# Kernel tuning notes

Measured on AMD Instinct MI355X. Metric: run time of the kernel, lower is better.

Reference implementation:

```python
import jax, jax.numpy as jnp
import numpy as np

N, K, D, E = 20000, 63, 50, 300  # nodes, neighbors per node, hidden dim, entity input dim


def setup_inputs() -> dict:
    key = jax.random.key(0)
    ks = jax.random.split(key, 12)
    inp = {
        "query_emb": jax.random.normal(ks[0], (N, D), jnp.float32),
        "entity_emb": jax.random.normal(ks[1], (N, E), jnp.float32),
        "neighbor_embs": jax.random.normal(ks[2], (N, K, D), jnp.float32),
        "neighbor_scores": jax.random.uniform(ks[3], (N, K + 1), jnp.float32),
        # learned parameters (xavier-ish scale)
        "Wp": jax.random.normal(ks[4], (D, E), jnp.float32) * (1.0 / np.sqrt(E)),
        "bp": jnp.zeros((D,), jnp.float32),
        "Wbil": jax.random.normal(ks[5], (D, D, D), jnp.float32) * (1.0 / D),
        "bbil": jnp.zeros((D,), jnp.float32),
        "Wg": jax.random.normal(ks[6], (D, D), jnp.float32) * (1.0 / np.sqrt(D)),
        "g_bias": jnp.zeros((D,), jnp.float32),
        "Wr": jax.random.normal(ks[7], (1, D), jnp.float32) * (1.0 / np.sqrt(D)),
        "br": jnp.zeros((1,), jnp.float32),
    }
    return inp


def reference(query_emb, entity_emb, neighbor_embs, neighbor_scores,
              Wp, bp, Wbil, bbil, Wg, g_bias, Wr, br):
    # entity projection: [N,E] -> [N,D]
    ent = entity_emb @ Wp.T + bp
    # bilinear query-entity interaction: node[n,o] = q[n,i] Wbil[o,i,j] ent[n,j] + bbil[o]
    node = jnp.einsum('ni,oij,nj->no', query_emb, Wbil, ent) + bbil  # [N,D]
    # ragged neighbor texts = K paraembeds + the node's own embedding (uniform K here)
    texts = jnp.concatenate([neighbor_embs, node[:, None, :]], axis=1)  # [N,K+1,D]
    # GRN: project neighbors, scale by attention scores, sum over neighbors
    # (dropout p=0.01 is identity in eval mode)
    proj = jnp.einsum('nkd,od->nko', texts, Wg)           # [N,K+1,D]
    agg = jnp.einsum('nko,nk->no', proj, neighbor_scores)  # attention-weighted scatter-sum
    feats = jax.nn.elu(agg + g_bias)                       # bias + ELU activation
    # rank score head: [N,D] -> [N,1]
    return feats @ Wr.T + br
```

## Files before the change

kernel.cpp:

```cpp
#include <hip/hip_runtime.h>
#include <math.h>

#define NN 20000
typedef unsigned int uint;
typedef unsigned short ushort;
typedef __attribute__((ext_vector_type(8))) short bf16x8;
typedef __attribute__((ext_vector_type(4))) float f32x4;

union U8 { uint4 u; bf16x8 v; };

__device__ __forceinline__ ushort f2b(float x) {
    uint u = __float_as_uint(x);
    return (ushort)((u + 0x7FFFu + ((u >> 16) & 1u)) >> 16);
}
__device__ __forceinline__ float b2f(ushort b) {
    return __uint_as_float(((uint)b) << 16);
}
__device__ __forceinline__ uint pkmul(uint e2, float qv) {
    float lo = __uint_as_float(e2 << 16) * qv;
    float hi = __uint_as_float(e2 & 0xFFFF0000u) * qv;
    uint ul = (__float_as_uint(lo) + 0x8000u) >> 16;
    uint uh = (__float_as_uint(hi) + 0x8000u) & 0xFFFF0000u;
    return ul | uh;
}

__global__ __launch_bounds__(256) void kPrep(const float* __restrict__ Wbil,
                                             const float* __restrict__ Wp,
                                             ushort* __restrict__ WtT2,
                                             ushort* __restrict__ WpB) {
    const int stride = gridDim.x * 256;
    for (int idx = blockIdx.x * 256 + threadIdx.x; idx < 64 * 3200; idx += stride) {
        int o = idx / 3200, k = idx - o * 3200;
        int i = k >> 6, j = k & 63;
        WtT2[idx] = (o < 50 && j < 50) ? f2b(Wbil[o * 2500 + i * 50 + j]) : (ushort)0;
    }
    for (int idx = blockIdx.x * 256 + threadIdx.x; idx < 64 * 384; idx += stride) {
        int d = idx / 384, e = idx - d * 384;
        WpB[idx] = (d < 50 && e < 300) ? f2b(Wp[d * 300 + e]) : (ushort)0;
    }
}

__global__ __launch_bounds__(256, 3) void kMain(
    const float* __restrict__ q,
    const float* __restrict__ entity,
    const float* __restrict__ bp,
    const ushort* __restrict__ WpB,
    const ushort* __restrict__ WtT2,
    float* __restrict__ part)
{
    __shared__ ushort qs[64 * 50];
    __shared__ ushort es[64 * 72];
    __shared__ ushort Bs[2][64 * 144];

    const int tid = threadIdx.x;
    const int h = blockIdx.x & 1;
    const int n0 = (blockIdx.x >> 1) * 64;
    const int w = tid >> 6, lane = tid & 63;
    const int c = lane & 15, quad = lane >> 4;
    const int nl = tid >> 2;
    const int kc = (tid & 3) * 32;
    const int myrow = w * 16 + c;

    for (int i = tid; i < 3200; i += 256) {
        int r = i / 50, d = i - r * 50;
        float v = (n0 + r < NN) ? q[(size_t)(n0 + r) * 50 + d] : 0.f;
        qs[i] = f2b(v);
    }

    ushort* BsE = &Bs[0][0];
    ushort* BsW = &Bs[1][0];
    f32x4 accE[4] = {{0.f,0.f,0.f,0.f},{0.f,0.f,0.f,0.f},{0.f,0.f,0.f,0.f},{0.f,0.f,0.f,0.f}};
    for (int t = 0; t < 3; ++t) {
        const int e0 = t * 128;
        __syncthreads();
        {
            const int node = n0 + nl;
            uint pk[16];
            #pragma unroll
            for (int u8 = 0; u8 < 8; ++u8) {
                const int e = e0 + kc + u8 * 4;
                float4 v = make_float4(0.f, 0.f, 0.f, 0.f);
                if (node < NN && e < 300)
                    v = *(const float4*)(entity + (size_t)node * 300 + e);
                pk[u8 * 2]     = (uint)f2b(v.x) | ((uint)f2b(v.y) << 16);
                pk[u8 * 2 + 1] = (uint)f2b(v.z) | ((uint)f2b(v.w) << 16);
            }
            uint4* dst = (uint4*)(BsE + nl * 144 + kc);
            #pragma unroll
            for (int m = 0; m < 4; ++m)
                dst[m] = make_uint4(pk[m*4], pk[m*4+1], pk[m*4+2], pk[m*4+3]);
        }
        {
            const uint4* src = (const uint4*)(WpB + nl * 384 + e0 + kc);
            uint4 v0 = src[0], v1 = src[1], v2 = src[2], v3 = src[3];
            uint4* dst = (uint4*)(BsW + nl * 144 + kc);
            dst[0] = v0; dst[1] = v1; dst[2] = v2; dst[3] = v3;
        }
        __syncthreads();
        #pragma unroll
        for (int ks = 0; ks < 4; ++ks) {
            bf16x8 a = *(const bf16x8*)(BsE + myrow * 144 + ks * 32 + quad * 8);
            #pragma unroll
            for (int nt = 0; nt < 4; ++nt) {
                bf16x8 b = *(const bf16x8*)(BsW + (nt * 16 + c) * 144 + ks * 32 + quad * 8);
                accE[nt] = __builtin_amdgcn_mfma_f32_16x16x32_bf16(a, b, accE[nt], 0, 0, 0);
            }
        }
    }
    #pragma unroll
    for (int nt = 0; nt < 4; ++nt) {
        const int d = nt * 16 + c;
        const float bias = (d < 50) ? bp[d] : 0.f;
        #pragma unroll
        for (int r = 0; r < 4; ++r) {
            const int row = w * 16 + quad * 4 + r;
            es[row * 72 + d] = (d < 50) ? f2b(accE[nt][r] + bias) : (ushort)0;
        }
    }
    const ushort* myes = es + myrow * 72;
    const uint4 es0 = *(const uint4*)(myes + quad * 8);
    const uint4 es1 = *(const uint4*)(myes + 32 + quad * 8);
    const ushort* qrow = qs + myrow * 50;

    const int kb0 = h ? 1664 : 0;
    const int ntiles = h ? 12 : 13;
    f32x4 acc[4] = {{0.f,0.f,0.f,0.f},{0.f,0.f,0.f,0.f},{0.f,0.f,0.f,0.f},{0.f,0.f,0.f,0.f}};

    __syncthreads();
    {
        const uint4* src = (const uint4*)(WtT2 + nl * 3200 + kb0 + kc);
        uint4 v0 = src[0], v1 = src[1], v2 = src[2], v3 = src[3];
        uint4* dst = (uint4*)(&Bs[0][0] + nl * 144 + kc);
        dst[0] = v0; dst[1] = v1; dst[2] = v2; dst[3] = v3;
    }
    __syncthreads();

    for (int t = 0; t < ntiles; ++t) {
        uint4 p0, p1, p2, p3;
        if (t + 1 < ntiles) {
            const uint4* src = (const uint4*)(WtT2 + nl * 3200 + kb0 + (t + 1) * 128 + kc);
            p0 = src[0]; p1 = src[1]; p2 = src[2]; p3 = src[3];
        }
        const ushort* Bcur = &Bs[t & 1][0];
        const int i0 = (kb0 >> 6) + 2 * t;
        #pragma unroll
        for (int ip = 0; ip < 2; ++ip) {
            const float qv = b2f(qrow[i0 + ip]);
            #pragma unroll
            for (int hf = 0; hf < 2; ++hf) {
                const uint4 eu = hf ? es1 : es0;
                U8 ua;
                ua.u = make_uint4(pkmul(eu.x, qv), pkmul(eu.y, qv),
                                  pkmul(eu.z, qv), pkmul(eu.w, qv));
                const int ko = ip * 64 + hf * 32 + quad * 8;
                #pragma unroll
                for (int nt = 0; nt < 4; ++nt) {
                    bf16x8 b = *(const bf16x8*)(Bcur + (nt * 16 + c) * 144 + ko);
                    acc[nt] = __builtin_amdgcn_mfma_f32_16x16x32_bf16(ua.v, b, acc[nt], 0, 0, 0);
                }
            }
        }
        if (t + 1 < ntiles) {
            uint4* dst = (uint4*)(&Bs[(t + 1) & 1][0] + nl * 144 + kc);
            dst[0] = p0; dst[1] = p1; dst[2] = p2; dst[3] = p3;
        }
        __syncthreads();
    }

    #pragma unroll
    for (int nt = 0; nt < 4; ++nt) {
        const int o = nt * 16 + c;
        #pragma unroll
        for (int r = 0; r < 4; ++r) {
            const int node = n0 + w * 16 + quad * 4 + r;
            if (node < NN)
                part[((size_t)h * NN + node) * 64 + o] = acc[nt][r];
        }
    }
}

__global__ __launch_bounds__(256) void kB(const float* __restrict__ nb,
                                          const float* __restrict__ scores,
                                          const float* __restrict__ part,
                                          const float* __restrict__ bbil,
                                          const float* __restrict__ Wg,
                                          const float* __restrict__ g_bias,
                                          const float* __restrict__ Wr,
                                          const float* __restrict__ br,
                                          float* __restrict__ out) {
    __shared__ float Wgs[50 * 51];
    __shared__ float scs[256];
    __shared__ float tv[4][52];

    const int tid = threadIdx.x;
    const int n0 = blockIdx.x * 4;
    for (int idx = tid; idx < 2500; idx += 256) {
        int o = idx / 50, d = idx - o * 50;
        Wgs[o * 51 + d] = Wg[idx];
    }
    scs[tid] = scores[(size_t)n0 * 64 + tid];
    __syncthreads();

    const int w = tid >> 6, lane = tid & 63;
    const int n = n0 + w;
    if (lane < 25) {
        const int d2 = lane * 2;
        const float* base = nb + (size_t)n * 3150 + d2;
        const float* sw = &scs[w * 64];
        float t0 = 0.f, t1 = 0.f;
        #pragma unroll 9
        for (int k = 0; k < 63; ++k) {
            const float2 v = *(const float2*)(base + k * 50);
            t0 += sw[k] * v.x; t1 += sw[k] * v.y;
        }
        const float2 p0 = *(const float2*)(part + (size_t)n * 64 + d2);
        const float2 p1 = *(const float2*)(part + ((size_t)NN + n) * 64 + d2);
        tv[w][d2]     = t0 + sw[63] * (p0.x + p1.x + bbil[d2]);
        tv[w][d2 + 1] = t1 + sw[63] * (p0.y + p1.y + bbil[d2 + 1]);
    }
    __syncthreads();

    float p = 0.f;
    if (lane < 50) {
        float a = g_bias[lane];
        const float* wrow = &Wgs[lane * 51];
        const float* twv = &tv[w][0];
        #pragma unroll 10
        for (int d = 0; d < 50; ++d) a += wrow[d] * twv[d];
        const float f = a > 0.f ? a : (__expf(a) - 1.f);
        p = f * Wr[lane];
    }
    #pragma unroll
    for (int off = 32; off; off >>= 1) p += __shfl_down(p, off);
    if (lane == 0) out[n] = p + br[0];
}

extern "C" void kernel_launch(void* const* d_in, const int* in_sizes, int n_in,
                              void* d_out, int out_size, void* d_ws, size_t ws_size,
                              hipStream_t stream) {
    const float* q_   = (const float*)d_in[0];
    const float* ent  = (const float*)d_in[1];
    const float* nb   = (const float*)d_in[2];
    const float* scr  = (const float*)d_in[3];
    const float* Wp   = (const float*)d_in[4];
    const float* bp   = (const float*)d_in[5];
    const float* Wb   = (const float*)d_in[6];
    const float* bb   = (const float*)d_in[7];
    const float* Wg   = (const float*)d_in[8];
    const float* gb   = (const float*)d_in[9];
    const float* Wr   = (const float*)d_in[10];
    const float* br   = (const float*)d_in[11];
    float* out = (float*)d_out;

    ushort* WtT2 = (ushort*)d_ws;
    ushort* WpB  = WtT2 + 64 * 3200;
    float*  part = (float*)(WpB + 64 * 384);

    hipLaunchKernelGGL(kPrep, dim3(256),  dim3(256), 0, stream, Wb, Wp, WtT2, WpB);
    hipLaunchKernelGGL(kMain, dim3(626),  dim3(256), 0, stream, q_, ent, bp, WpB, WtT2, part);
    hipLaunchKernelGGL(kB,    dim3(5000), dim3(256), 0, stream, nb, scr, part, bb, Wg, gb, Wr, br, out);
}
```

Before: 437.6 us.

## Split entity projection into separate kernel and widen neighbor aggregation to 8 nodes/block

```diff
diff --git a/kernel.cpp b/kernel.cpp
--- a/kernel.cpp
+++ b/kernel.cpp
@@ -16,12 +16,10 @@
 __device__ __forceinline__ float b2f(ushort b) {
     return __uint_as_float(((uint)b) << 16);
 }
-__device__ __forceinline__ uint pkmul(uint e2, float qv) {
-    float lo = __uint_as_float(e2 << 16) * qv;
-    float hi = __uint_as_float(e2 & 0xFFFF0000u) * qv;
-    uint ul = (__float_as_uint(lo) + 0x8000u) >> 16;
-    uint uh = (__float_as_uint(hi) + 0x8000u) & 0xFFFF0000u;
-    return ul | uh;
+__device__ __forceinline__ uint cvt_pk_bf16(float lo, float hi) {
+    uint r;
+    asm("v_cvt_pk_bf16_f32 %0, %1, %2" : "=v"(r) : "v"(lo), "v"(hi));
+    return r;
 }
 
 __global__ __launch_bounds__(256) void kPrep(const float* __restrict__ Wbil,
@@ -40,16 +38,78 @@
     }
 }
 
+__global__ __launch_bounds__(256) void kEnt(const float* __restrict__ entity,
+                                            const float* __restrict__ bp,
+                                            const ushort* __restrict__ WpB,
+                                            float* __restrict__ entG) {
+    __shared__ ushort BsE[64 * 144];
+    __shared__ ushort BsW[64 * 144];
+    const int tid = threadIdx.x;
+    const int n0 = blockIdx.x * 64;
+    const int w = tid >> 6, lane = tid & 63;
+    const int c = lane & 15, quad = lane >> 4;
+    const int nl = tid >> 2;
+    const int kc = (tid & 3) * 32;
+    const int myrow = w * 16 + c;
+
+    f32x4 accE[4] = {{0.f,0.f,0.f,0.f},{0.f,0.f,0.f,0.f},{0.f,0.f,0.f,0.f},{0.f,0.f,0.f,0.f}};
+    for (int t = 0; t < 3; ++t) {
+        const int e0 = t * 128;
+        __syncthreads();
+        {
+            const int node = n0 + nl;
+            uint pk[16];
+            #pragma unroll
+            for (int u8 = 0; u8 < 8; ++u8) {
+                const int e = e0 + kc + u8 * 4;
+                float4 v = make_float4(0.f, 0.f, 0.f, 0.f);
+                if (node < NN && e < 300)
+                    v = *(const float4*)(entity + (size_t)node * 300 + e);
+                pk[u8 * 2]     = cvt_pk_bf16(v.x, v.y);
+                pk[u8 * 2 + 1] = cvt_pk_bf16(v.z, v.w);
+            }
+            uint4* dst = (uint4*)(BsE + nl * 144 + kc);
+            #pragma unroll
+            for (int m = 0; m < 4; ++m)
+                dst[m] = make_uint4(pk[m*4], pk[m*4+1], pk[m*4+2], pk[m*4+3]);
+        }
+        {
+            const uint4* src = (const uint4*)(WpB + nl * 384 + e0 + kc);
+            uint4 v0 = src[0], v1 = src[1], v2 = src[2], v3 = src[3];
+            uint4* dst = (uint4*)(BsW + nl * 144 + kc);
+            dst[0] = v0; dst[1] = v1; dst[2] = v2; dst[3] = v3;
+        }
+        __syncthreads();
+        #pragma unroll
+        for (int ks = 0; ks < 4; ++ks) {
+            bf16x8 a = *(const bf16x8*)(BsE + myrow * 144 + ks * 32 + quad * 8);
+            #pragma unroll
+            for (int nt = 0; nt < 4; ++nt) {
+                bf16x8 b = *(const bf16x8*)(BsW + (nt * 16 + c) * 144 + ks * 32 + quad * 8);
+                accE[nt] = __builtin_amdgcn_mfma_f32_16x16x32_bf16(a, b, accE[nt], 0, 0, 0);
+            }
+        }
+    }
+    #pragma unroll
+    for (int nt = 0; nt < 4; ++nt) {
+        const int o = nt * 16 + c;
+        const float bias = (o < 50) ? bp[o] : 0.f;
+        #pragma unroll
+        for (int r = 0; r < 4; ++r) {
+            const int node = n0 + w * 16 + quad * 4 + r;
+            if (node < NN)
+                entG[(size_t)node * 64 + o] = (o < 50) ? (accE[nt][r] + bias) : 0.f;
+        }
+    }
+}
+
 __global__ __launch_bounds__(256, 3) void kMain(
     const float* __restrict__ q,
-    const float* __restrict__ entity,
-    const float* __restrict__ bp,
-    const ushort* __restrict__ WpB,
+    const float* __restrict__ entG,
     const ushort* __restrict__ WtT2,
     float* __restrict__ part)
 {
     __shared__ ushort qs[64 * 50];
-    __shared__ ushort es[64 * 72];
     __shared__ ushort Bs[2][64 * 144];
 
     const int tid = threadIdx.x;
@@ -67,66 +127,26 @@
         qs[i] = f2b(v);
     }
 
-    ushort* BsE = &Bs[0][0];
-    ushort* BsW = &Bs[1][0];
-    f32x4 accE[4] = {{0.f,0.f,0.f,0.f},{0.f,0.f,0.f,0.f},{0.f,0.f,0.f,0.f},{0.f,0.f,0.f,0.f}};
-    for (int t = 0; t < 3; ++t) {
-        const int e0 = t * 128;
-        __syncthreads();
-        {
-            const int node = n0 + nl;
-            uint pk[16];
-            #pragma unroll
-            for (int u8 = 0; u8 < 8; ++u8) {
-                const int e = e0 + kc + u8 * 4;
-                float4 v = make_float4(0.f, 0.f, 0.f, 0.f);
-                if (node < NN && e < 300)
-                    v = *(const float4*)(entity + (size_t)node * 300 + e);
-                pk[u8 * 2]     = (uint)f2b(v.x) | ((uint)f2b(v.y) << 16);
-                pk[u8 * 2 + 1] = (uint)f2b(v.z) | ((uint)f2b(v.w) << 16);
-            }
-            uint4* dst = (uint4*)(BsE + nl * 144 + kc);
-            #pragma unroll
-            for (int m = 0; m < 4; ++m)
-                dst[m] = make_uint4(pk[m*4], pk[m*4+1], pk[m*4+2], pk[m*4+3]);
-        }
-        {
-            const uint4* src = (const uint4*)(WpB + nl * 384 + e0 + kc);
-            uint4 v0 = src[0], v1 = src[1], v2 = src[2], v3 = src[3];
-            uint4* dst = (uint4*)(BsW + nl * 144 + kc);
-            dst[0] = v0; dst[1] = v1; dst[2] = v2; dst[3] = v3;
-        }
-        __syncthreads();
-        #pragma unroll
-        for (int ks = 0; ks < 4; ++ks) {
-            bf16x8 a = *(const bf16x8*)(BsE + myrow * 144 + ks * 32 + quad * 8);
-            #pragma unroll
-            for (int nt = 0; nt < 4; ++nt) {
-                bf16x8 b = *(const bf16x8*)(BsW + (nt * 16 + c) * 144 + ks * 32 + quad * 8);
-                accE[nt] = __builtin_amdgcn_mfma_f32_16x16x32_bf16(a, b, accE[nt], 0, 0, 0);
-            }
-        }
-    }
-    #pragma unroll
-    for (int nt = 0; nt < 4; ++nt) {
-        const int d = nt * 16 + c;
-        const float bias = (d < 50) ? bp[d] : 0.f;
-        #pragma unroll
-        for (int r = 0; r < 4; ++r) {
-            const int row = w * 16 + quad * 4 + r;
-            es[row * 72 + d] = (d < 50) ? f2b(accE[nt][r] + bias) : (ushort)0;
-        }
-    }
-    const ushort* myes = es + myrow * 72;
-    const uint4 es0 = *(const uint4*)(myes + quad * 8);
-    const uint4 es1 = *(const uint4*)(myes + 32 + quad * 8);
+    const int mynode = n0 + myrow;
+    float ef[16];
+    {
+        float4 a0 = make_float4(0.f,0.f,0.f,0.f), a1 = a0, b0 = a0, b1 = a0;
+        if (mynode < NN) {
+            const float4* ep = (const float4*)(entG + (size_t)mynode * 64 + quad * 8);
+            a0 = ep[0]; a1 = ep[1];
+            b0 = ep[8]; b1 = ep[9];
+        }
+        ef[0]=a0.x;  ef[1]=a0.y;  ef[2]=a0.z;  ef[3]=a0.w;
+        ef[4]=a1.x;  ef[5]=a1.y;  ef[6]=a1.z;  ef[7]=a1.w;
+        ef[8]=b0.x;  ef[9]=b0.y;  ef[10]=b0.z; ef[11]=b0.w;
+        ef[12]=b1.x; ef[13]=b1.y; ef[14]=b1.z; ef[15]=b1.w;
+    }
     const ushort* qrow = qs + myrow * 50;
 
     const int kb0 = h ? 1664 : 0;
     const int ntiles = h ? 12 : 13;
     f32x4 acc[4] = {{0.f,0.f,0.f,0.f},{0.f,0.f,0.f,0.f},{0.f,0.f,0.f,0.f},{0.f,0.f,0.f,0.f}};
 
-    __syncthreads();
     {
         const uint4* src = (const uint4*)(WtT2 + nl * 3200 + kb0 + kc);
         uint4 v0 = src[0], v1 = src[1], v2 = src[2], v3 = src[3];
@@ -148,10 +168,12 @@
             const float qv = b2f(qrow[i0 + ip]);
             #pragma unroll
             for (int hf = 0; hf < 2; ++hf) {
-                const uint4 eu = hf ? es1 : es0;
+                const float* e = ef + hf * 8;
                 U8 ua;
-                ua.u = make_uint4(pkmul(eu.x, qv), pkmul(eu.y, qv),
-                                  pkmul(eu.z, qv), pkmul(eu.w, qv));
+                ua.u = make_uint4(cvt_pk_bf16(e[0] * qv, e[1] * qv),
+                                  cvt_pk_bf16(e[2] * qv, e[3] * qv),
+                                  cvt_pk_bf16(e[4] * qv, e[5] * qv),
+                                  cvt_pk_bf16(e[6] * qv, e[7] * qv));
                 const int ko = ip * 64 + hf * 32 + quad * 8;
                 #pragma unroll
                 for (int nt = 0; nt < 4; ++nt) {
@@ -189,24 +211,31 @@
                                           const float* __restrict__ br,
                                           float* __restrict__ out) {
     __shared__ float Wgs[50 * 51];
-    __shared__ float scs[256];
-    __shared__ float tv[4][52];
+    __shared__ float scs[512];
+    __shared__ float tv[8][52];
+    __shared__ float cb[8][64];
 
     const int tid = threadIdx.x;
-    const int n0 = blockIdx.x * 4;
+    const int n0 = blockIdx.x * 8;
+
     for (int idx = tid; idx < 2500; idx += 256) {
         int o = idx / 50, d = idx - o * 50;
         Wgs[o * 51 + d] = Wg[idx];
     }
-    scs[tid] = scores[(size_t)n0 * 64 + tid];
+    scs[tid]       = scores[(size_t)n0 * 64 + tid];
+    scs[tid + 256] = scores[(size_t)n0 * 64 + 256 + tid];
+    ((float*)cb)[tid] = 0.f;
+    ((float*)cb)[tid + 256] = 0.f;
     __syncthreads();
 
     const int w = tid >> 6, lane = tid & 63;
-    const int n = n0 + w;
-    if (lane < 25) {
-        const int d2 = lane * 2;
+    const int half = lane >> 5, l = lane & 31;
+    const int ni = 2 * w + half;
+    const int n = n0 + ni;
+    if (l < 25) {
+        const int d2 = l * 2;
         const float* base = nb + (size_t)n * 3150 + d2;
-        const float* sw = &scs[w * 64];
+        const float* sw = &scs[ni * 64];
         float t0 = 0.f, t1 = 0.f;
         #pragma unroll 9
         for (int k = 0; k < 63; ++k) {
@@ -215,24 +244,27 @@
         }
         const float2 p0 = *(const float2*)(part + (size_t)n * 64 + d2);
         const float2 p1 = *(const float2*)(part + ((size_t)NN + n) * 64 + d2);
-        tv[w][d2]     = t0 + sw[63] * (p0.x + p1.x + bbil[d2]);
-        tv[w][d2 + 1] = t1 + sw[63] * (p0.y + p1.y + bbil[d2 + 1]);
-    }
-    __syncthreads();
-
-    float p = 0.f;
-    if (lane < 50) {
-        float a = g_bias[lane];
-        const float* wrow = &Wgs[lane * 51];
-        const float* twv = &tv[w][0];
+        tv[ni][d2]     = t0 + sw[63] * (p0.x + p1.x + bbil[d2]);
+        tv[ni][d2 + 1] = t1 + sw[63] * (p0.y + p1.y + bbil[d2 + 1]);
+    }
+    __syncthreads();
+
+    for (int p = tid; p < 400; p += 256) {
+        const int n2 = p / 50, o = p - n2 * 50;
+        const float* wrow = &Wgs[o * 51];
+        const float* twv = &tv[n2][0];
+        float a = g_bias[o];
         #pragma unroll 10
         for (int d = 0; d < 50; ++d) a += wrow[d] * twv[d];
         const float f = a > 0.f ? a : (__expf(a) - 1.f);
-        p = f * Wr[lane];
-    }
+        cb[n2][o] = f * Wr[o];
+    }
+    __syncthreads();
+
+    float v = cb[ni][l] + cb[ni][l + 32];
     #pragma unroll
-    for (int off = 32; off; off >>= 1) p += __shfl_down(p, off);
-    if (lane == 0) out[n] = p + br[0];
+    for (int off = 16; off; off >>= 1) v += __shfl_xor(v, off);
+    if (l == 0) out[n] = v + br[0];
 }
 
 extern "C" void kernel_launch(void* const* d_in, const int* in_sizes, int n_in,
@@ -254,9 +286,11 @@
 
     ushort* WtT2 = (ushort*)d_ws;
     ushort* WpB  = WtT2 + 64 * 3200;
-    float*  part = (float*)(WpB + 64 * 384);
+    float*  entG = (float*)(WpB + 64 * 384);
+    float*  part = entG + (size_t)NN * 64;
 
     hipLaunchKernelGGL(kPrep, dim3(256),  dim3(256), 0, stream, Wb, Wp, WtT2, WpB);
-    hipLaunchKernelGGL(kMain, dim3(626),  dim3(256), 0, stream, q_, ent, bp, WpB, WtT2, part);
-    hipLaunchKernelGGL(kB,    dim3(5000), dim3(256), 0, stream, nb, scr, part, bb, Wg, gb, Wr, br, out);
-}
+    hipLaunchKernelGGL(kEnt,  dim3(313),  dim3(256), 0, stream, ent, bp, WpB, entG);
+    hipLaunchKernelGGL(kMain, dim3(626),  dim3(256), 0, stream, q_, entG, WtT2, part);
+    hipLaunchKernelGGL(kB,    dim3(2500), dim3(256), 0, stream, nb, scr, part, bb, Wg, gb, Wr, br, out);
+}
```

New measurement: 430.0 us, median of 2. About the same (-1.7%).
